# Performance work log

Hardware: AMD Instinct MI355X
Metric: run time of the kernel (lower is better)

The kernel has to match this reference:

```python
import jax, jax.numpy as jnp
import numpy as np

DIM = 512
HEADS = 4
HEAD_DIM = DIM // HEADS
SCALE = HEAD_DIM ** -0.5


def _lin(x, W, b):
    # torch nn.Linear: y = x @ W.T + b, W is [out, in]
    return jnp.einsum('...i,oi->...o', x, W) + b


def setup_inputs() -> dict:
    key = jax.random.key(0)
    ks = jax.random.split(key, 20)
    f1 = jax.random.normal(ks[0], (4, 5, DIM, 10, 10), dtype=jnp.float32)
    f2 = jax.random.normal(ks[1], (4, 75, DIM, 10, 10), dtype=jnp.float32)
    names = ['k1', 'v1', 'q2', 'k2', 'v2', 'o1', 'o2']
    inp = {'f1': f1, 'f2': f2}
    for i, nm in enumerate(names):
        inp['W' + nm] = 0.02 * jax.random.normal(ks[2 + 2 * i], (DIM, DIM), dtype=jnp.float32)
        inp['b' + nm] = 0.02 * jax.random.normal(ks[3 + 2 * i], (DIM,), dtype=jnp.float32)
    return inp


def _forward(f1, f2, Wk1, bk1, Wv1, bv1, Wq2, bq2, Wk2, bk2, Wv2, bv2, Wo1, bo1, Wo2, bo2):
    B, n1, C, H, W = f1.shape
    n2 = f2.shape[1]
    L = H * W
    # [B,n,C,H,W] -> [B,n,L,C]
    f1t = f1.reshape(B, n1, C, L).transpose(0, 1, 3, 2)
    f2t = f2.reshape(B, n2, C, L).transpose(0, 1, 3, 2)

    def split_heads(x, n):  # [B,n,L,C] -> [B,heads,n*L,hd]
        return x.reshape(B, n * L, HEADS, HEAD_DIM).transpose(0, 2, 1, 3)

    def merge_heads(x, n):  # [B,heads,n*L,hd] -> [B,n,L,C]
        return x.transpose(0, 2, 1, 3).reshape(B, n, L, C)

    K1 = split_heads(_lin(f1t, Wk1, bk1), n1)
    V1 = split_heads(_lin(f1t, Wv1, bv1), n1)
    Q2 = split_heads(_lin(f2t, Wq2, bq2), n2)
    K2 = split_heads(_lin(f2t, Wk2, bk2), n2)  # computed as in original, unused downstream
    V2 = split_heads(_lin(f2t, Wv2, bv2), n2)

    # Query attends to support: [B,h,n2*L,n1*L]
    att_q = jax.nn.softmax(jnp.einsum('bhqd,bhkd->bhqk', Q2, K1) * SCALE, axis=-1)
    out2 = jnp.einsum('bhqk,bhkd->bhqd', att_q, V1)
    out2 = _lin(merge_heads(out2, n2), Wo2, bo2)
    out2 = out2.transpose(0, 1, 3, 2).reshape(B, n2, C, H, W)

    # Support attends to query: [B,h,n1*L,n2*L]
    att_s = jax.nn.softmax(jnp.einsum('bhsd,bhqd->bhsq', K1, Q2) * SCALE, axis=-1)
    out1 = jnp.einsum('bhsq,bhqd->bhsd', att_s, V2)
    out1 = _lin(merge_heads(out1, n1), Wo1, bo1)
    out1 = out1.transpose(0, 1, 3, 2).reshape(B, n1, C, H, W)
    return (out1, out2)


def reference(f1, f2, Wk1, bk1, Wv1, bv1, Wq2, bq2, Wk2, bk2, Wv2, bv2, Wo1, bo1, Wo2, bo2):
    return _forward(f1, f2, Wk1, bk1, Wv1, bv1, Wq2, bq2, Wk2, bk2, Wv2, bv2, Wo1, bo1, Wo2, bo2)
```

## Files before the change

kernel.cpp:

```cpp
#include <hip/hip_runtime.h>
#include <hip/hip_bf16.h>


#define QSCL  (0.08838834764831845f * 1.4426950408889634f)
#define KSPL  8
#define NRB2  59
#define NRB1  4

using bf16x8 = __attribute__((ext_vector_type(8))) short;
using f32x4  = __attribute__((ext_vector_type(4))) float;

__device__ inline ushort f2bf(float x) {
    union { float f; unsigned u; } v; v.f = x;
    unsigned r = v.u + 0x7fff + ((v.u >> 16) & 1);
    return (ushort)(r >> 16);
}

__device__ inline void gll16(const ushort* g, ushort* l) {
    __builtin_amdgcn_global_load_lds(
        (const __attribute__((address_space(1))) void*)g,
        (__attribute__((address_space(3))) void*)l, 16, 0, 0);
}

struct PreArgs { const float* w[6]; float s[6]; const float* f1; const float* f2; };

__global__ __launch_bounds__(256) void pre_kernel(
    PreArgs pa, ushort* __restrict__ Wb,
    ushort* __restrict__ f1t, ushort* __restrict__ f2t)
{
    __shared__ ushort Ts[100 * 136];
    const int t   = threadIdx.x;
    const int bid = blockIdx.x;

    if (bid < 1536) {
        const int wsel = bid >> 8;
        const float* src = pa.w[wsel];
        const float sc = pa.s[wsel];
        ushort* d = Wb + (size_t)wsel * 262144;
        const int idx = ((bid & 255) * 256 + t) * 4;
        const float4 v = *(const float4*)(src + idx);
        ushort4 o;
        o.x = f2bf(v.x * sc); o.y = f2bf(v.y * sc);
        o.z = f2bf(v.z * sc); o.w = f2bf(v.w * sc);
        *(ushort4*)(d + idx) = o;
        return;
    }

    const int bn = bid - 1536;
    const float* Xb;
    ushort* Yb;
    if (bn < 20) { Xb = pa.f1 + (size_t)bn * 51200;        Yb = f1t + (size_t)bn * 51200; }
    else         { Xb = pa.f2 + (size_t)(bn - 20) * 51200; Yb = f2t + (size_t)(bn - 20) * 51200; }

    for (int c0 = 0; c0 < 512; c0 += 128) {
        __syncthreads();
        #pragma unroll
        for (int i = 0; i < 50; ++i) {
            const int id = i * 256 + t;
            const int c = id / 100, l = id - c * 100;
            Ts[l * 136 + c] = f2bf(Xb[(size_t)(c0 + c) * 100 + l]);
        }
        __syncthreads();
        #pragma unroll
        for (int i = 0; i < 7; ++i) {
            const int id = i * 256 + t;
            if (id < 1600) {
                const int cg = id & 15, l = id >> 4;
                *(uint4*)(Yb + (size_t)l * 512 + c0 + cg * 8) =
                    *(const uint4*)&Ts[l * 136 + cg * 8];
            }
        }
    }
}

struct GemmJob {
    const ushort* A; const ushort* B;
    const float* bias; void* C;
    size_t sA, sB, sC;
    float bscale;
    int ldC, Mrows, Ncols, gx, gy, fastn, baxis, nblk;
};

struct GemmJobs { GemmJob j0, j1, j2, j3; int ntot; };

template<int EPI>
__global__ __launch_bounds__(256) void gemm_nt(GemmJobs J)
{
    __shared__ ushort smem[17408];
    ushort* As = smem;
    ushort* Bs = smem + 8192;

    const int ntot = J.ntot;
    const int q8 = ntot >> 3, r8 = ntot & 7;
    const int xcd = blockIdx.x & 7, ii = blockIdx.x >> 3;
    const int work = (xcd < r8 ? xcd * (q8 + 1)
                               : r8 * (q8 + 1) + (xcd - r8) * q8) + ii;

    GemmJob j; int id;
    {
        const int c0 = J.j0.nblk;
        const int c1 = c0 + J.j1.nblk;
        const int c2 = c1 + J.j2.nblk;
        if (work < c0)      { j = J.j0; id = work; }
        else if (work < c1) { j = J.j1; id = work - c0; }
        else if (work < c2) { j = J.j2; id = work - c1; }
        else                { j = J.j3; id = work - c2; }
    }

    const int fx = id % j.gx;
    const int rem = id / j.gx;
    const int fy = rem % j.gy;
    const int bz = rem / j.gy;
    const int m0 = (j.fastn ? fy : fx) * 128;
    const int n0 = (j.fastn ? fx : fy) * 128;

    const int t    = threadIdx.x;
    const int lane = t & 63;
    const int w    = t >> 6;
    const int mw   = (w >> 1) * 64;
    const int nw   = (w & 1) * 64;
    const int Mrows = j.Mrows, Ncols = j.Ncols, ldC = j.ldC;
    const ushort* Ab = j.A + (size_t)bz * j.sA;
    const ushort* Bb = j.B + (size_t)bz * j.sB;
    const float* bias = j.bias;

    f32x4 acc[4][4];
    #pragma unroll
    for (int i = 0; i < 4; ++i)
        #pragma unroll
        for (int jj = 0; jj < 4; ++jj) acc[i][jj] = (f32x4){0.f, 0.f, 0.f, 0.f};

    const int lr = lane >> 3;
    const int cb = lane & 7;

    for (int k0 = 0; k0 < 512; k0 += 64) {
        if (k0) __syncthreads();
        #pragma unroll
        for (int i = 0; i < 4; ++i) {
            const int row = w * 32 + i * 8 + lr;
            const int ar = min(m0 + row, Mrows - 1);
            gll16(Ab + (size_t)ar * 512 + k0 + ((cb ^ (row & 7)) * 8),
                  As + (w * 32 + i * 8) * 64);
            const int br = min(n0 + row, Ncols - 1);
            gll16(Bb + (size_t)br * 512 + k0 + ((cb ^ (row & 7)) * 8),
                  Bs + (w * 32 + i * 8) * 64);
        }
        __syncthreads();
        #pragma unroll
        for (int ks = 0; ks < 2; ++ks) {
            bf16x8 af[4], bv[4];
            #pragma unroll
            for (int mf = 0; mf < 4; ++mf) {
                const int row = mw + mf * 16 + (lane & 15);
                af[mf] = *(const bf16x8*)((const char*)As + row * 128 +
                          ((ks * 64 + (lane >> 4) * 16) ^ ((row & 7) << 4)));
            }
            #pragma unroll
            for (int nf = 0; nf < 4; ++nf) {
                const int row = nw + nf * 16 + (lane & 15);
                bv[nf] = *(const bf16x8*)((const char*)Bs + row * 128 +
                          ((ks * 64 + (lane >> 4) * 16) ^ ((row & 7) << 4)));
            }
            #pragma unroll
            for (int mf = 0; mf < 4; ++mf)
                #pragma unroll
                for (int nf = 0; nf < 4; ++nf)
                    acc[mf][nf] = __builtin_amdgcn_mfma_f32_16x16x32_bf16(
                        af[mf], bv[nf], acc[mf][nf], 0, 0, 0);
        }
    }
    __syncthreads();

    if (EPI == 0) {
        float bcol[4];
        if (j.baxis == 1) {
            #pragma unroll
            for (int nf = 0; nf < 4; ++nf)
                bcol[nf] = bias[n0 + nw + nf * 16 + (lane & 15)] * j.bscale;
        }
        ushort* Ts = smem;
        #pragma unroll
        for (int mf = 0; mf < 4; ++mf) {
            #pragma unroll
            for (int r = 0; r < 4; ++r) {
                const int row = mw + mf * 16 + (lane >> 4) * 4 + r;
                const float brow = (j.baxis == 0) ? bias[m0 + row] * j.bscale : 0.f;
                #pragma unroll
                for (int nf = 0; nf < 4; ++nf) {
                    const int col = nw + nf * 16 + (lane & 15);
                    const float v = acc[mf][nf][r] +
                                    ((j.baxis == 1) ? bcol[nf] : brow);
                    Ts[row * 136 + col] = f2bf(v);
                }
            }
        }
        __syncthreads();
        ushort* Cb = (ushort*)j.C + (size_t)bz * j.sC;
        #pragma unroll
        for (int i = 0; i < 8; ++i) {
            const int id2 = i * 256 + t;
            const int row = id2 >> 4, cg = id2 & 15;
            if (m0 + row < Mrows)
                *(uint4*)(Cb + (size_t)(m0 + row) * ldC + n0 + cg * 8) =
                    *(const uint4*)&Ts[row * 136 + cg * 8];
        }
    } else {
        float* Ts2 = (float*)smem;
        float* Cb = (float*)j.C + (size_t)bz * j.sC;
        const int colL = t & 127;
        const int rb2 = t >> 7;
        const int tg = n0 + colL;
        int nIdx = 0, lIdx = 0;
        if (tg < Ncols) { nIdx = tg / 100; lIdx = tg - nIdx * 100; }
        #pragma unroll
        for (int h = 0; h < 2; ++h) {
            __syncthreads();
            if ((mw >> 6) == h) {
                #pragma unroll
                for (int mf = 0; mf < 4; ++mf) {
                    #pragma unroll
                    for (int r = 0; r < 4; ++r) {
                        const int rowl = mf * 16 + (lane >> 4) * 4 + r;
                        const float brow = bias[m0 + h * 64 + rowl];
                        #pragma unroll
                        for (int nf = 0; nf < 4; ++nf) {
                            const int col = nw + nf * 16 + (lane & 15);
                            Ts2[rowl * 132 + col] = acc[mf][nf][r] + brow;
                        }
                    }
                }
            }
            __syncthreads();
            if (tg < Ncols) {
                float* dst = Cb + (size_t)nIdx * 51200 + lIdx;
                #pragma unroll
                for (int i = 0; i < 32; ++i) {
                    const int rowl = i * 2 + rb2;
                    const int c = m0 + h * 64 + rowl;
                    dst[(size_t)c * 100] = Ts2[rowl * 132 + colL];
                }
            }
        }
    }
}

__global__ __launch_bounds__(256, 2) void attn_mfma_kernel(
    const ushort* __restrict__ Q2, const ushort* __restrict__ K1,
    const ushort* __restrict__ V1t, const ushort* __restrict__ V2t,
    ushort* __restrict__ A2, float* __restrict__ PartO, float* __restrict__ Pml)
{
    __shared__ ushort Ks[2 * 64 * 128];
    __shared__ ushort Vs[2 * 128 * 64];

    const int t    = threadIdx.x;
    const int lane = t & 63;
    const int w    = t >> 6;

    const int flat = blockIdx.x;
    const int xcd = flat & 7, ii = flat >> 3;
    const bool dir2 = (ii >= 64);
    int rb, h, b, sp = 0;
    if (dir2) {
        const int w2 = xcd * 118 + (ii - 64);
        rb = w2 % NRB2;
        const int hb = w2 / NRB2;
        h = hb & 3; b = hb >> 2;
    } else {
        const int w1 = xcd * 64 + ii;
        rb = w1 & 3; sp = (w1 >> 2) & 7;
        const int hb = w1 >> 5;
        h = hb & 3; b = hb >> 2;
    }

    const int TR = dir2 ? 7500 : 500;
    const int TK = dir2 ? 500 : 7500;
    const int strideV = dir2 ? 512 : 7552;
    const ushort* R  = dir2 ? Q2 : K1;
    const ushort* Kt = dir2 ? K1 : Q2;
    const ushort* Vt = dir2 ? V1t : V2t;

    const int r0 = rb * 128;
    const int ho = h * 128;

    int kbeg = 0, kend = TK;
    if (!dir2) {
        kbeg = sp * 938;
        kend = kbeg + 938; if (kend > TK) kend = TK;
    }

    bf16x8 qa0[4], qa1[4];
    {
        const ushort* Rb = R + (size_t)b * TR * 512;
        const int q0 = min(r0 + w * 32 + (lane & 15), TR - 1);
        const int q1 = min(r0 + w * 32 + 16 + (lane & 15), TR - 1);
        const ushort* qp0 = Rb + (size_t)q0 * 512 + ho + (lane >> 4) * 8;
        const ushort* qp1 = Rb + (size_t)q1 * 512 + ho + (lane >> 4) * 8;
        #pragma unroll
        for (int s = 0; s < 4; ++s) {
            qa0[s] = *(const bf16x8*)(qp0 + s * 32);
            qa1[s] = *(const bf16x8*)(qp1 + s * 32);
        }
    }

    const ushort* Kb = Kt + (size_t)b * TK * 512;
    const ushort* Vb = Vt + ((size_t)b * 512 + ho) * strideV;

    const int krow_i = lane >> 4;
    const int kcol   = (lane & 15) * 8;
    const int vrow_i = lane >> 3;
    const int vcol   = (lane & 7) * 8;
    const int gq     = lane >> 4;

    float m_run0 = -3.0e38f, l_run0 = 0.f;
    float m_run1 = -3.0e38f, l_run1 = 0.f;
    f32x4 acc0[8], acc1[8];
    #pragma unroll
    for (int g = 0; g < 8; ++g) {
        acc0[g] = (f32x4){0.f, 0.f, 0.f, 0.f};
        acc1[g] = (f32x4){0.f, 0.f, 0.f, 0.f};
    }

    #pragma unroll
    for (int i = 0; i < 4; ++i) {
        const int kr = w * 16 + i * 4 + krow_i;
        gll16(Kb + (size_t)(kbeg + kr) * 512 + ho + (kcol ^ ((kr & 7) << 3)),
              Ks + (w * 16 + i * 4) * 128);
        const int vd = w * 32 + i * 8 + vrow_i;
        gll16(Vb + (size_t)vd * strideV + kbeg + (vcol ^ ((vd & 7) << 3)),
              Vs + (w * 32 + i * 8) * 64);
    }
    asm volatile("s_waitcnt vmcnt(0)" ::: "memory");
    __builtin_amdgcn_s_barrier();
    __builtin_amdgcn_sched_barrier(0);

    int c = 0;
    for (int kbase = kbeg; kbase < kend; kbase += 64, ++c) {
        const ushort* KsC = Ks + (c & 1) * 8192;
        const ushort* VsC = Vs + (c & 1) * 8192;
        ushort* KsN = Ks + ((c + 1) & 1) * 8192;
        ushort* VsN = Vs + ((c + 1) & 1) * 8192;

        const int kn = kbase + 64;
        if (kn < kend) {
            #pragma unroll
            for (int i = 0; i < 4; ++i) {
                const int kr = w * 16 + i * 4 + krow_i;
                gll16(Kb + (size_t)(kn + kr) * 512 + ho + (kcol ^ ((kr & 7) << 3)),
                      KsN + (w * 16 + i * 4) * 128);
                const int vd = w * 32 + i * 8 + vrow_i;
                gll16(Vb + (size_t)vd * strideV + kn + (vcol ^ ((vd & 7) << 3)),
                      VsN + (w * 32 + i * 8) * 64);
            }
        }

        f32x4 sf0[4], sf1[4];
        __builtin_amdgcn_s_setprio(1);
        #pragma unroll
        for (int f = 0; f < 4; ++f) {
            f32x4 s0 = (f32x4){0.f, 0.f, 0.f, 0.f};
            f32x4 s1 = (f32x4){0.f, 0.f, 0.f, 0.f};
            const int kr = f * 16 + (lane & 15);
            const int kb2 = kr * 256, sw = (kr & 7) << 4, g16 = gq * 16;
            #pragma unroll
            for (int s4 = 0; s4 < 4; ++s4) {
                bf16x8 kf = *(const bf16x8*)((const char*)KsC + kb2 + ((s4 * 64 + g16) ^ sw));
                s0 = __builtin_amdgcn_mfma_f32_16x16x32_bf16(kf, qa0[s4], s0, 0, 0, 0);
                s1 = __builtin_amdgcn_mfma_f32_16x16x32_bf16(kf, qa1[s4], s1, 0, 0, 0);
            }
            sf0[f] = s0; sf1[f] = s1;
        }
        __builtin_amdgcn_s_setprio(0);

        if (kbase + 64 > kend) {
            #pragma unroll
            for (int f = 0; f < 4; ++f)
                #pragma unroll
                for (int r = 0; r < 4; ++r)
                    if (kbase + f * 16 + gq * 4 + r >= kend) {
                        sf0[f][r] = -3.0e38f; sf1[f][r] = -3.0e38f;
                    }
        }
        {
            float mx = sf0[0][0];
            #pragma unroll
            for (int f = 0; f < 4; ++f)
                #pragma unroll
                for (int r = 0; r < 4; ++r) mx = fmaxf(mx, sf0[f][r]);
            mx = fmaxf(mx, __shfl_xor(mx, 16));
            mx = fmaxf(mx, __shfl_xor(mx, 32));
            if (__any(mx > m_run0 + 11.0f)) {
                const float mn = fmaxf(m_run0, mx);
                const float sc = __builtin_amdgcn_exp2f(m_run0 - mn);
                m_run0 = mn; l_run0 *= sc;
                float scal4[4];
                #pragma unroll
                for (int r = 0; r < 4; ++r)
                    scal4[r] = __shfl(sc, (lane & 48) + gq * 4 + r);
                #pragma unroll
                for (int g = 0; g < 8; ++g)
                    #pragma unroll
                    for (int r = 0; r < 4; ++r) acc0[g][r] *= scal4[r];
            }
            float rs = 0.f;
            #pragma unroll
            for (int f = 0; f < 4; ++f)
                #pragma unroll
                for (int r = 0; r < 4; ++r) {
                    const float p = __builtin_amdgcn_exp2f(sf0[f][r] - m_run0);
                    sf0[f][r] = p; rs += p;
                }
            rs += __shfl_xor(rs, 16);
            rs += __shfl_xor(rs, 32);
            l_run0 += rs;
        }
        {
            float mx = sf1[0][0];
            #pragma unroll
            for (int f = 0; f < 4; ++f)
                #pragma unroll
                for (int r = 0; r < 4; ++r) mx = fmaxf(mx, sf1[f][r]);
            mx = fmaxf(mx, __shfl_xor(mx, 16));
            mx = fmaxf(mx, __shfl_xor(mx, 32));
            if (__any(mx > m_run1 + 11.0f)) {
                const float mn = fmaxf(m_run1, mx);
                const float sc = __builtin_amdgcn_exp2f(m_run1 - mn);
                m_run1 = mn; l_run1 *= sc;
                float scal4[4];
                #pragma unroll
                for (int r = 0; r < 4; ++r)
                    scal4[r] = __shfl(sc, (lane & 48) + gq * 4 + r);
                #pragma unroll
                for (int g = 0; g < 8; ++g)
                    #pragma unroll
                    for (int r = 0; r < 4; ++r) acc1[g][r] *= scal4[r];
            }
            float rs = 0.f;
            #pragma unroll
            for (int f = 0; f < 4; ++f)
                #pragma unroll
                for (int r = 0; r < 4; ++r) {
                    const float p = __builtin_amdgcn_exp2f(sf1[f][r] - m_run1);
                    sf1[f][r] = p; rs += p;
                }
            rs += __shfl_xor(rs, 16);
            rs += __shfl_xor(rs, 32);
            l_run1 += rs;
        }

        union { uint u[4]; bf16x8 v; } pa00, pa01, pa10, pa11;
        {
            uint pk0[4][2], pk1[4][2];
            #pragma unroll
            for (int f = 0; f < 4; ++f) {
                asm("v_cvt_pk_bf16_f32 %0, %1, %2" : "=v"(pk0[f][0]) : "v"(sf0[f][0]), "v"(sf0[f][1]));
                asm("v_cvt_pk_bf16_f32 %0, %1, %2" : "=v"(pk0[f][1]) : "v"(sf0[f][2]), "v"(sf0[f][3]));
                asm("v_cvt_pk_bf16_f32 %0, %1, %2" : "=v"(pk1[f][0]) : "v"(sf1[f][0]), "v"(sf1[f][1]));
                asm("v_cvt_pk_bf16_f32 %0, %1, %2" : "=v"(pk1[f][1]) : "v"(sf1[f][2]), "v"(sf1[f][3]));
            }
            #pragma unroll
            for (int u = 0; u < 4; ++u) {
                const int srcl = (lane & 15) + ((lane & 16) << 1) + ((u >> 1) << 4);
                const uint a0 = (uint)__shfl((int)pk0[0][u & 1], srcl);
                const uint b0 = (uint)__shfl((int)pk0[1][u & 1], srcl);
                const uint a1 = (uint)__shfl((int)pk0[2][u & 1], srcl);
                const uint b1 = (uint)__shfl((int)pk0[3][u & 1], srcl);
                pa00.u[u] = (lane & 32) ? b0 : a0;
                pa01.u[u] = (lane & 32) ? b1 : a1;
                const uint c0 = (uint)__shfl((int)pk1[0][u & 1], srcl);
                const uint d0 = (uint)__shfl((int)pk1[1][u & 1], srcl);
                const uint c1 = (uint)__shfl((int)pk1[2][u & 1], srcl);
                const uint d1 = (uint)__shfl((int)pk1[3][u & 1], srcl);
                pa10.u[u] = (lane & 32) ? d0 : c0;
                pa11.u[u] = (lane & 32) ? d1 : c1;
            }
        }

        {
            const int g16 = gq * 16;
            __builtin_amdgcn_s_setprio(1);
            #pragma unroll
            for (int g = 0; g < 8; ++g) {
                const int dr = g * 16 + (lane & 15);
                const int vb = dr * 128, vsw = (dr & 7) << 4;
                bf16x8 v0 = *(const bf16x8*)((const char*)VsC + vb + ((g16) ^ vsw));
                bf16x8 v1 = *(const bf16x8*)((const char*)VsC + vb + ((64 + g16) ^ vsw));
                acc0[g] = __builtin_amdgcn_mfma_f32_16x16x32_bf16(pa00.v, v0, acc0[g], 0, 0, 0);
                acc0[g] = __builtin_amdgcn_mfma_f32_16x16x32_bf16(pa01.v, v1, acc0[g], 0, 0, 0);
                acc1[g] = __builtin_amdgcn_mfma_f32_16x16x32_bf16(pa10.v, v0, acc1[g], 0, 0, 0);
                acc1[g] = __builtin_amdgcn_mfma_f32_16x16x32_bf16(pa11.v, v1, acc1[g], 0, 0, 0);
            }
            __builtin_amdgcn_s_setprio(0);
        }

        asm volatile("s_waitcnt vmcnt(0)" ::: "memory");
        __builtin_amdgcn_s_barrier();
        __builtin_amdgcn_sched_barrier(0);
    }

    if (dir2) {
        float linv0[4], linv1[4];
        #pragma unroll
        for (int r = 0; r < 4; ++r) {
            linv0[r] = 1.f / __shfl(l_run0, (lane & 48) + gq * 4 + r);
            linv1[r] = 1.f / __shfl(l_run1, (lane & 48) + gq * 4 + r);
        }
        #pragma unroll
        for (int r = 0; r < 4; ++r) {
            const int row0 = r0 + w * 32 + (gq << 2) + r;
            if (row0 < TR) {
                ushort* Ab2 = A2 + ((size_t)b * TR + row0) * 512 + ho + (lane & 15);
                #pragma unroll
                for (int g = 0; g < 8; ++g) Ab2[g * 16] = f2bf(acc0[g][r] * linv0[r]);
            }
            const int row1 = r0 + w * 32 + 16 + (gq << 2) + r;
            if (row1 < TR) {
                ushort* Ab2 = A2 + ((size_t)b * TR + row1) * 512 + ho + (lane & 15);
                #pragma unroll
                for (int g = 0; g < 8; ++g) Ab2[g * 16] = f2bf(acc1[g][r] * linv1[r]);
            }
        }
    } else {
        const size_t tile = (((size_t)b * 4 + h) * NRB1 + rb) * KSPL + sp;
        float* Po = PartO + tile * (128 * 128);
        float* Pm = Pml + tile * 256;
        #pragma unroll
        for (int r = 0; r < 4; ++r) {
            const int row0 = w * 32 + (gq << 2) + r;
            float* pp0 = Po + row0 * 128 + (lane & 15);
            #pragma unroll
            for (int g = 0; g < 8; ++g) pp0[g * 16] = acc0[g][r];
            const int row1 = w * 32 + 16 + (gq << 2) + r;
            float* pp1 = Po + row1 * 128 + (lane & 15);
            #pragma unroll
            for (int g = 0; g < 8; ++g) pp1[g * 16] = acc1[g][r];
        }
        if (lane < 16) {
            Pm[w * 32 + lane] = m_run0;
            Pm[w * 32 + 16 + lane] = m_run1;
            Pm[128 + w * 32 + lane] = l_run0;
            Pm[128 + w * 32 + 16 + lane] = l_run1;
        }
    }
}

__global__ __launch_bounds__(256) void attn_combine_kernel(
    const float* __restrict__ PartO, const float* __restrict__ Pml,
    ushort* __restrict__ Aout, int TR)
{
    const int t = threadIdx.x;
    const int rb = blockIdx.x >> 1, half = blockIdx.x & 1;
    const int h = blockIdx.y, b = blockIdx.z;
    const int row = half * 64 + (t >> 2);
    const int dq = (t & 3) * 32;
    const int r0 = rb * 128;
    const size_t tbase = (((size_t)b * 4 + h) * NRB1 + rb) * KSPL;

    float M = -3.0e38f;
    #pragma unroll
    for (int i = 0; i < KSPL; ++i)
        M = fmaxf(M, Pml[(tbase + i) * 256 + row]);
    float wt[KSPL], L = 0.f;
    #pragma unroll
    for (int i = 0; i < KSPL; ++i) {
        const float wi = __builtin_amdgcn_exp2f(Pml[(tbase + i) * 256 + row] - M);
        wt[i] = wi;
        L += wi * Pml[(tbase + i) * 256 + 128 + row];
    }
    if (r0 + row >= TR) return;
    const float invL = 1.f / L;

    float o[32];
    #pragma unroll
    for (int j = 0; j < 32; ++j) o[j] = 0.f;
    #pragma unroll
    for (int i = 0; i < KSPL; ++i) {
        const float* pp = PartO + (tbase + i) * (128 * 128) + row * 128 + dq;
        #pragma unroll
        for (int j = 0; j < 32; j += 4) {
            const float4 v = *(const float4*)(pp + j);
            o[j] += wt[i] * v.x; o[j+1] += wt[i] * v.y;
            o[j+2] += wt[i] * v.z; o[j+3] += wt[i] * v.w;
        }
    }
    ushort* Ab = Aout + ((size_t)b * TR + r0 + row) * 512 + h * 128 + dq;
    #pragma unroll
    for (int j = 0; j < 32; j += 4) {
        ushort4 v;
        v.x = f2bf(o[j] * invL); v.y = f2bf(o[j+1] * invL);
        v.z = f2bf(o[j+2] * invL); v.w = f2bf(o[j+3] * invL);
        *(ushort4*)(Ab + j) = v;
    }
}

extern "C" void kernel_launch(void* const* d_in, const int* in_sizes, int n_in,
                              void* d_out, int out_size, void* d_ws, size_t ws_size,
                              hipStream_t stream) {
    const float* f1  = (const float*)d_in[0];
    const float* f2  = (const float*)d_in[1];
    const float* Wk1 = (const float*)d_in[2];
    const float* bk1 = (const float*)d_in[3];
    const float* Wv1 = (const float*)d_in[4];
    const float* bv1 = (const float*)d_in[5];
    const float* Wq2 = (const float*)d_in[6];
    const float* bq2 = (const float*)d_in[7];
    const float* Wv2 = (const float*)d_in[10];
    const float* bv2 = (const float*)d_in[11];
    const float* Wo1 = (const float*)d_in[12];
    const float* bo1 = (const float*)d_in[13];
    const float* Wo2 = (const float*)d_in[14];
    const float* bo2 = (const float*)d_in[15];
    float* out = (float*)d_out;

    ushort* f1t = (ushort*)d_ws;
    ushort* f2t = f1t + (size_t)1024000;
    ushort* Wb  = f2t + (size_t)15360000;
    ushort* K1  = Wb  + (size_t)1572864;
    ushort* Q2  = K1  + (size_t)1024000;
    ushort* V1t = Q2  + (size_t)15360000;
    ushort* V2t = V1t + (size_t)1048576;
    ushort* A1  = V2t + (size_t)15466496;
    ushort* A2  = A1  + (size_t)1024000;
    float* PartO = (float*)(A2 + (size_t)15360000);
    float* Pml   = PartO + (size_t)512*128*128;

    const dim3 blk(256);

    const ushort* Wk1b = Wb;
    const ushort* Wv1b = Wb + 262144;
    const ushort* Wq2b = Wb + 2*262144;
    const ushort* Wv2b = Wb + 3*262144;
    const ushort* Wo1b = Wb + 4*262144;
    const ushort* Wo2b = Wb + 5*262144;

    PreArgs pa;
    pa.w[0]=Wk1; pa.w[1]=Wv1; pa.w[2]=Wq2; pa.w[3]=Wv2; pa.w[4]=Wo1; pa.w[5]=Wo2;
    pa.s[0]=1.f; pa.s[1]=1.f; pa.s[2]=QSCL; pa.s[3]=1.f; pa.s[4]=1.f; pa.s[5]=1.f;
    pa.f1 = f1; pa.f2 = f2;
    pre_kernel<<<dim3(1856), blk, 0, stream>>>(pa, Wb, f1t, f2t);

    GemmJob jK {f1t, Wk1b, bk1, K1, 0, 0, 0, 1.f, 512, 2000, 512,
                4, 16, 1, 1, 64};
    GemmJob jQ {f2t, Wq2b, bq2, Q2, 0, 0, 0, QSCL, 512, 30000, 512,
                4, 235, 1, 1, 940};
    GemmJob jV1{Wv1b, f1t, bv1, V1t, 0, (size_t)500*512, (size_t)512*512, 1.f,
                512, 512, 500, 4, 4, 0, 0, 64};
    GemmJob jV2{Wv2b, f2t, bv2, V2t, 0, (size_t)7500*512, (size_t)512*7552, 1.f,
                7552, 512, 7500, 4, 59, 0, 0, 944};
    GemmJobs JP{jK, jQ, jV1, jV2, 2012};
    gemm_nt<0><<<dim3(2012), blk, 0, stream>>>(JP);

    attn_mfma_kernel<<<dim3(1456), dim3(256), 0, stream>>>(
        Q2, K1, V1t, V2t, A2, PartO, Pml);
    attn_combine_kernel<<<dim3(8, 4, 4), blk, 0, stream>>>(PartO, Pml, A1, 500);

    GemmJob jO1{Wo1b, A1, bo1, out, 0, (size_t)500*512, (size_t)5*51200, 1.f,
                0, 512, 500, 4, 4, 0, 0, 64};
    GemmJob jO2{Wo2b, A2, bo2, out + (size_t)1024000, 0, (size_t)7500*512,
                (size_t)75*51200, 1.f, 0, 512, 7500, 4, 59, 0, 0, 944};
    GemmJob jZ{};
    GemmJobs JO{jO1, jO2, jZ, jZ, 1008};
    gemm_nt<2><<<dim3(1008), blk, 0, stream>>>(JO);
}
```

Baseline: 232.3 us.

## Halve dir1 key splits, vectorize input transpose loads, stage A2 stores via LDS

The support-to-query attention now uses 4 key-range splits instead of 8. This cuts the number of partial outputs and shrinks the attention grid, but each dir1 block gets longer. The transpose in pre_kernel reads float4 vectors instead of scalar floats. The dir2 epilogue writes normalized bf16 outputs into LDS and then emits coalesced 16-byte stores instead of scattered 2-byte global writes, which adds one barrier.

```diff
diff --git a/kernel.cpp b/kernel.cpp
--- a/kernel.cpp
+++ b/kernel.cpp
@@ -3,7 +3,7 @@
 
 
 #define QSCL  (0.08838834764831845f * 1.4426950408889634f)
-#define KSPL  8
+#define KSPL  4
 #define NRB2  59
 #define NRB1  4
 
@@ -55,10 +55,17 @@
     for (int c0 = 0; c0 < 512; c0 += 128) {
         __syncthreads();
         #pragma unroll
-        for (int i = 0; i < 50; ++i) {
+        for (int i = 0; i < 13; ++i) {
             const int id = i * 256 + t;
-            const int c = id / 100, l = id - c * 100;
-            Ts[l * 136 + c] = f2bf(Xb[(size_t)(c0 + c) * 100 + l]);
+            if (id < 3200) {
+                const int c = id / 25, q = id - c * 25;
+                const float4 v = *(const float4*)(Xb + (size_t)(c0 + c) * 100 + q * 4);
+                const int base = (q * 4) * 136 + c;
+                Ts[base]       = f2bf(v.x);
+                Ts[base + 136] = f2bf(v.y);
+                Ts[base + 272] = f2bf(v.z);
+                Ts[base + 408] = f2bf(v.w);
+            }
         }
         __syncthreads();
         #pragma unroll
@@ -258,17 +265,17 @@
 
     const int flat = blockIdx.x;
     const int xcd = flat & 7, ii = flat >> 3;
-    const bool dir2 = (ii >= 64);
+    const bool dir2 = (ii >= 32);
     int rb, h, b, sp = 0;
     if (dir2) {
-        const int w2 = xcd * 118 + (ii - 64);
+        const int w2 = xcd * 118 + (ii - 32);
         rb = w2 % NRB2;
         const int hb = w2 / NRB2;
         h = hb & 3; b = hb >> 2;
     } else {
-        const int w1 = xcd * 64 + ii;
-        rb = w1 & 3; sp = (w1 >> 2) & 7;
-        const int hb = w1 >> 5;
+        const int w1 = xcd * 32 + ii;
+        rb = w1 & 3; sp = (w1 >> 2) & 3;
+        const int hb = w1 >> 4;
         h = hb & 3; b = hb >> 2;
     }
 
@@ -284,8 +291,8 @@
 
     int kbeg = 0, kend = TK;
     if (!dir2) {
-        kbeg = sp * 938;
-        kend = kbeg + 938; if (kend > TK) kend = TK;
+        kbeg = sp * 1875;
+        kend = kbeg + 1875; if (kend > TK) kend = TK;
     }
 
     bf16x8 qa0[4], qa1[4];
@@ -504,20 +511,26 @@
             linv0[r] = 1.f / __shfl(l_run0, (lane & 48) + gq * 4 + r);
             linv1[r] = 1.f / __shfl(l_run1, (lane & 48) + gq * 4 + r);
         }
+        ushort* Ts = Ks;
         #pragma unroll
         for (int r = 0; r < 4; ++r) {
-            const int row0 = r0 + w * 32 + (gq << 2) + r;
-            if (row0 < TR) {
-                ushort* Ab2 = A2 + ((size_t)b * TR + row0) * 512 + ho + (lane & 15);
-                #pragma unroll
-                for (int g = 0; g < 8; ++g) Ab2[g * 16] = f2bf(acc0[g][r] * linv0[r]);
-            }
-            const int row1 = r0 + w * 32 + 16 + (gq << 2) + r;
-            if (row1 < TR) {
-                ushort* Ab2 = A2 + ((size_t)b * TR + row1) * 512 + ho + (lane & 15);
-                #pragma unroll
-                for (int g = 0; g < 8; ++g) Ab2[g * 16] = f2bf(acc1[g][r] * linv1[r]);
-            }
+            const int rl0 = w * 32 + (gq << 2) + r;
+            const int rl1 = rl0 + 16;
+            #pragma unroll
+            for (int g = 0; g < 8; ++g) {
+                Ts[rl0 * 128 + g * 16 + (lane & 15)] = f2bf(acc0[g][r] * linv0[r]);
+                Ts[rl1 * 128 + g * 16 + (lane & 15)] = f2bf(acc1[g][r] * linv1[r]);
+            }
+        }
+        __syncthreads();
+        #pragma unroll
+        for (int i = 0; i < 8; ++i) {
+            const int id = i * 256 + t;
+            const int row = id >> 4, cg = id & 15;
+            const int grow = r0 + row;
+            if (grow < TR)
+                *(uint4*)(A2 + ((size_t)b * TR + grow) * 512 + ho + cg * 8) =
+                    *(const uint4*)&Ts[row * 128 + cg * 8];
         }
     } else {
         const size_t tile = (((size_t)b * 4 + h) * NRB1 + rb) * KSPL + sp;
@@ -621,7 +634,7 @@
     ushort* A1  = V2t + (size_t)15466496;
     ushort* A2  = A1  + (size_t)1024000;
     float* PartO = (float*)(A2 + (size_t)15360000);
-    float* Pml   = PartO + (size_t)512*128*128;
+    float* Pml   = PartO + (size_t)256*128*128;
 
     const dim3 blk(256);
 
@@ -649,7 +662,7 @@
     GemmJobs JP{jK, jQ, jV1, jV2, 2012};
     gemm_nt<0><<<dim3(2012), blk, 0, stream>>>(JP);
 
-    attn_mfma_kernel<<<dim3(1456), dim3(256), 0, stream>>>(
+    attn_mfma_kernel<<<dim3(1200), dim3(256), 0, stream>>>(
         Q2, K1, V1t, V2t, A2, PartO, Pml);
     attn_combine_kernel<<<dim3(8, 4, 4), blk, 0, stream>>>(PartO, Pml, A1, 500);
 
```

Measured after the change: 250.8 us. 1.08x slower.
